# Performance work log

Hardware: AMD Instinct MI355X
Metric: run time of the kernel (lower is better)

## Reference

```python
import jax, jax.numpy as jnp
import numpy as np

D_MODEL = 1024
N_HEADS = 16
D_HEAD = D_MODEL // N_HEADS
BATCH = 2
SEQ = 2048


def setup_inputs() -> dict:
    key = jax.random.key(0)
    ks = jax.random.split(key, 16)
    s = 0.02
    d = D_MODEL
    return {
        "x": jax.random.normal(ks[0], (BATCH, SEQ, d), jnp.float32),
        "Wq": jax.random.normal(ks[1], (d, d), jnp.float32) * s,
        "bq": jnp.zeros((d,), jnp.float32),
        "Wk": jax.random.normal(ks[2], (d, d), jnp.float32) * s,
        "bk": jnp.zeros((d,), jnp.float32),
        "Wv": jax.random.normal(ks[3], (d, d), jnp.float32) * s,
        "bv": jnp.zeros((d,), jnp.float32),
        "Wo": jax.random.normal(ks[4], (d, d), jnp.float32) * s,
        "bo": jnp.zeros((d,), jnp.float32),
        "Wt": jax.random.normal(ks[5], (d, 1), jnp.float32) * s,
        "bt": jnp.zeros((1,), jnp.float32),
        "Wg": jax.random.normal(ks[6], (d, d), jnp.float32) * s,
        "bg": jnp.zeros((d,), jnp.float32),
    }


def _evolved_attention(x, Wq, bq, Wk, bk, Wv, bv, Wo, bo, Wt, bt, Wg, bg):
    B, S, D = x.shape
    H, dh = N_HEADS, D_HEAD

    def heads(y):  # [B,S,D] -> [B,H,S,dh]
        return y.reshape(B, S, H, dh).transpose(0, 2, 1, 3)

    q = heads(x @ Wq + bq)
    k = heads(x @ Wk + bk)
    v = heads(x @ Wv + bv)

    # cosine similarity (F.normalize with eps=1e-12)
    qn = q / jnp.maximum(jnp.linalg.norm(q, axis=-1, keepdims=True), 1e-12)
    kn = k / jnp.maximum(jnp.linalg.norm(k, axis=-1, keepdims=True), 1e-12)
    scores = jnp.einsum("bhqd,bhkd->bhqk", qn, kn)

    # adaptive temperature: sigmoid(temp_proj(mean_s x)) + 0.5, shape [B,1]
    temp = jax.nn.sigmoid(x.mean(axis=1) @ Wt + bt) + 0.5  # [B,1]
    scores = scores / temp[:, None, None, :]  # broadcast [B,1,1,1]

    # sparsemax-style: softmax over top-k (k = S//4), scattered back
    kk = max(1, S // 4)
    vals, idx = jax.lax.top_k(scores, kk)          # [B,H,S,kk]
    w = jax.nn.softmax(vals, axis=-1)
    rows = jnp.arange(B * H * S)[:, None]
    attn = (
        jnp.zeros((B * H * S, S), scores.dtype)
        .at[rows, idx.reshape(-1, kk)]
        .set(w.reshape(-1, kk))
        .reshape(B, H, S, S)
    )

    out = jnp.einsum("bhqk,bhkd->bhqd", attn, v)
    out = out.transpose(0, 2, 1, 3).reshape(B, S, D)
    out = out @ Wo + bo

    # highway gating
    gate = jax.nn.sigmoid(x @ Wg + bg)
    return gate * out + (1.0 - gate) * x


def reference(x, Wq, bq, Wk, bk, Wv, bv, Wo, bo, Wt, bt, Wg, bg):
    return _evolved_attention(x, Wq, bq, Wk, bk, Wv, bv, Wo, bo, Wt, bt, Wg, bg)
```

## Files before the change

### kernel.cpp

```cpp
#include <hip/hip_runtime.h>

typedef unsigned short u16;
typedef __attribute__((ext_vector_type(4))) float f32x4;
typedef __attribute__((ext_vector_type(8))) short bf16x8;
typedef __attribute__((ext_vector_type(4))) int i32x4;

#define BB 2
#define SS 2048
#define DD 1024
#define HH 16
#define DH 64
#define KK 512

#define OFF_SCAL  ((size_t)0)
#define OFF_WT    ((size_t)256)
#define OFF_XB    (OFF_WT + (size_t)5*1024*1024*2)
#define OFF_AO    OFF_XB
#define OFF_QH    (OFF_XB + (size_t)4096*1024*2)
#define OFF_QN    (OFF_QH + (size_t)4096*4096*2)
#define OFF_KN    (OFF_QN + (size_t)4096*1024*2)
#define OFF_VT    (OFF_KN + (size_t)4096*1024*2)

__device__ __forceinline__ float b2f(u16 u) { return __uint_as_float(((unsigned)u) << 16); }
__device__ __forceinline__ u16 f2b(float f) {
    unsigned u = __float_as_uint(f);
    return (u16)((u + 0x7fffu + ((u >> 16) & 1u)) >> 16);
}

__device__ __forceinline__ void gload16(const u16* g, u16* l) {
    __builtin_amdgcn_global_load_lds(
        (__attribute__((address_space(1))) void*)g,
        (__attribute__((address_space(3))) void*)l, 16, 0, 0);
}

__global__ __launch_bounds__(256) void convert_x(const float* x, u16* xb) {
    int i = (blockIdx.x * 256 + threadIdx.x) * 4;
    float4 v = *(const float4*)(x + i);
    u16 r0 = f2b(v.x), r1 = f2b(v.y), r2 = f2b(v.z), r3 = f2b(v.w);
    xb[i] = r0; xb[i + 1] = r1; xb[i + 2] = r2; xb[i + 3] = r3;
}

__global__ __launch_bounds__(256) void transpose_w(
        const float* Wq, const float* Wk, const float* Wv, const float* Wg, const float* Wo,
        u16* WT) {
    int z = blockIdx.z;
    const float* src = (z == 0) ? Wq : (z == 1) ? Wk : (z == 2) ? Wv : (z == 3) ? Wg : Wo;
    u16* dst = WT + (size_t)z * 1024 * 1024;
    __shared__ float tile[64][65];
    int n0 = blockIdx.x * 64, k0 = blockIdx.y * 64;
    int rbase = threadIdx.x >> 6, c = threadIdx.x & 63;
#pragma unroll
    for (int i = 0; i < 16; i++) {
        int r = i * 4 + rbase;
        tile[r][c] = src[(size_t)(k0 + r) * 1024 + n0 + c];
    }
    __syncthreads();
#pragma unroll
    for (int i = 0; i < 16; i++) {
        int r = i * 4 + rbase;
        dst[(size_t)(n0 + r) * 1024 + k0 + c] = f2b(tile[c][r]);
    }
}

__global__ __launch_bounds__(256) void temp_partial(const float* x, const float* Wt,
                                                    float* accbuf) {
    int b = blockIdx.x >> 5, ch = blockIdx.x & 31;
    float a = 0.f;
    for (int si = 0; si < 64; si++) {
        int s = ch * 64 + si;
        const float* xr = x + ((size_t)(b * SS + s)) * DD;
#pragma unroll
        for (int k = 0; k < 4; k++) {
            int c = threadIdx.x + k * 256;
            a += xr[c] * Wt[c];
        }
    }
    for (int o = 32; o; o >>= 1) a += __shfl_xor(a, o);
    __shared__ float red[4];
    if ((threadIdx.x & 63) == 0) red[threadIdx.x >> 6] = a;
    __syncthreads();
    if (threadIdx.x == 0) atomicAdd(&accbuf[b], red[0] + red[1] + red[2] + red[3]);
}

__global__ void temp_final(const float* accbuf, const float* bt, float* itemp) {
    int t = threadIdx.x;
    if (t < BB) {
        float v = accbuf[t] / (float)SS + bt[0];
        float tmp = 1.f / (1.f + __expf(-v)) + 0.5f;
        itemp[t] = 1.f / tmp;
    }
}

__global__ __launch_bounds__(256) void gemm_qkvg(
        const u16* X, const u16* WT,
        const float* bq, const float* bk, const float* bv, const float* bg, u16* Qh) {
    __shared__ __align__(16) u16 la[128 * 32];
    __shared__ __align__(16) u16 lb[128 * 32];
    int tid = threadIdx.x, wid = tid >> 6, lane = tid & 63;
    int quad = lane >> 4, ml = lane & 15;
    int m0 = blockIdx.x * 128, n0 = blockIdx.y * 128;
    int wr = wid >> 1, wc = wid & 1;

    f32x4 acc[4][4];
#pragma unroll
    for (int i = 0; i < 4; i++)
#pragma unroll
        for (int j = 0; j < 4; j++) acc[i][j] = (f32x4){0.f, 0.f, 0.f, 0.f};

    int t0 = wid * 2, t1 = t0 + 1;
    int r0 = lane >> 2, kp = lane & 3;
    const u16* ga0 = X + (size_t)(m0 + t0 * 16 + r0) * 1024 + kp * 8;
    const u16* ga1 = X + (size_t)(m0 + t1 * 16 + r0) * 1024 + kp * 8;
    const u16* gb0 = WT + (size_t)(n0 + t0 * 16 + r0) * 1024 + kp * 8;
    const u16* gb1 = WT + (size_t)(n0 + t1 * 16 + r0) * 1024 + kp * 8;
    u16* la0 = la + t0 * 512; u16* la1 = la + t1 * 512;
    u16* lb0 = lb + t0 * 512; u16* lb1 = lb + t1 * 512;

    for (int k0 = 0; k0 < 1024; k0 += 32) {
        gload16(ga0 + k0, la0);
        gload16(ga1 + k0, la1);
        gload16(gb0 + k0, lb0);
        gload16(gb1 + k0, lb1);
        __syncthreads();
        bf16x8 af[4], bfr[4];
#pragma unroll
        for (int mi = 0; mi < 4; mi++)
            af[mi] = *(const bf16x8*)&la[(wr * 64 + mi * 16 + ml) * 32 + quad * 8];
#pragma unroll
        for (int ni = 0; ni < 4; ni++)
            bfr[ni] = *(const bf16x8*)&lb[(wc * 64 + ni * 16 + ml) * 32 + quad * 8];
#pragma unroll
        for (int mi = 0; mi < 4; mi++)
#pragma unroll
            for (int ni = 0; ni < 4; ni++)
                acc[mi][ni] = __builtin_amdgcn_mfma_f32_16x16x32_bf16(af[mi], bfr[ni],
                                                                      acc[mi][ni], 0, 0, 0);
        __syncthreads();
    }

#pragma unroll
    for (int mi = 0; mi < 4; mi++)
#pragma unroll
        for (int ni = 0; ni < 4; ni++) {
            int col = n0 + wc * 64 + ni * 16 + ml;
            int mat = col >> 10, bc = col & 1023;
            const float* bp = (mat == 0) ? bq : (mat == 1) ? bk : (mat == 2) ? bv : bg;
            float bias = bp[bc];
#pragma unroll
            for (int r = 0; r < 4; r++) {
                int row = m0 + wr * 64 + mi * 16 + quad * 4 + r;
                Qh[(size_t)row * 4096 + col] = f2b(acc[mi][ni][r] + bias);
            }
        }
}

__global__ __launch_bounds__(256) void norm_repack(const u16* Qh, u16* qn, u16* kn, u16* vt) {
    int wid = threadIdx.x >> 6, lane = threadIdx.x & 63;
    int idx = blockIdx.x * 4 + wid;
    int token = idx >> 4, h = idx & 15;
    int b = token >> 11, s = token & 2047;
    int bh = b * HH + h;
    const u16* rowp = Qh + (size_t)token * 4096 + h * 64;
    float q = b2f(rowp[lane]);
    float k = b2f(rowp[1024 + lane]);
    u16 v = rowp[2048 + lane];
    float sq = q * q, sk = k * k;
    for (int o = 32; o; o >>= 1) { sq += __shfl_xor(sq, o); sk += __shfl_xor(sk, o); }
    float qd = fmaxf(sqrtf(sq), 1e-12f), kd = fmaxf(sqrtf(sk), 1e-12f);
    qn[((size_t)bh * SS + s) * DH + lane] = f2b(q / qd);
    kn[((size_t)bh * SS + s) * DH + lane] = f2b(k / kd);
    vt[((size_t)bh * DH + lane) * SS + s] = v;
}

#define EST 2088

__global__ __launch_bounds__(1024, 8) void attn_kernel(
        const u16* qn, const u16* kn, const u16* vt, const float* itemp, u16* ao) {
    __shared__ __align__(16) u16 e16[16 * EST];
    __shared__ float pvp[3][16][66];
    __shared__ float zrow_s[16];

    int tid = threadIdx.x, wid = tid >> 6, lane = tid & 63;
    int quad = lane >> 4, nl = lane & 15;
    int bh = blockIdx.x >> 7, qt = blockIdx.x & 127;
    int b = bh >> 4, h = bh & 15;
    const u16* qbase = qn + ((size_t)bh * SS + qt * 16) * DH;
    const u16* kbase = kn + (size_t)bh * SS * DH;
    const u16* vbase = vt + (size_t)bh * DH * SS;
    float it = itemp[b];

    bf16x8 aq0 = *(const bf16x8*)(qbase + nl * DH + quad * 8);
    bf16x8 aq1 = *(const bf16x8*)(qbase + nl * DH + 32 + quad * 8);

#pragma unroll 4
    for (int c = 0; c < 8; c++) {
        int j = c * 256 + wid * 16 + nl;
        const u16* kr = kbase + (size_t)j * DH;
        bf16x8 b0 = *(const bf16x8*)(kr + quad * 8);
        bf16x8 b1 = *(const bf16x8*)(kr + 32 + quad * 8);
        f32x4 acc = (f32x4){0.f, 0.f, 0.f, 0.f};
        acc = __builtin_amdgcn_mfma_f32_16x16x32_bf16(aq0, b0, acc, 0, 0, 0);
        acc = __builtin_amdgcn_mfma_f32_16x16x32_bf16(aq1, b1, acc, 0, 0, 0);
#pragma unroll
        for (int r = 0; r < 4; r++) e16[(quad * 4 + r) * EST + j] = f2b(acc[r] * it);
    }
    __syncthreads();

    {
        int row = wid;
        u16* rp = &e16[row * EST];
        int kk[32];
#pragma unroll
        for (int i = 0; i < 4; i++) {
            i32x4 kv = *(const i32x4*)(rp + i * 512 + lane * 8);
#pragma unroll
            for (int j = 0; j < 4; j++) {
                int r2 = kv[j];
                int t = ((r2 >> 15) & 0x00010001) * 0x7FFF;
                int key2 = r2 ^ 0x80008000 ^ t;
                kk[i * 8 + j * 2]     = key2 & 0xFFFF;
                kk[i * 8 + j * 2 + 1] = ((unsigned)key2) >> 16;
            }
        }
#pragma unroll
        for (int c = 0; c < 32; c++) asm volatile("" : "+v"(kk[c]));

        int P = 0;
        for (int bit = 15; bit >= 0; bit--) {
            int cand = P | (1 << bit);
            int cnt = 0;
#pragma unroll
            for (int c = 0; c < 32; c++)
                cnt += (int)__popcll(__ballot(kk[c] >= cand));
            if (cnt >= KK) P = cand;
            if (cnt == KK) break;
        }

        float z = 0.f;
#pragma unroll
        for (int i = 0; i < 4; i++) {
            i32x4 ev;
#pragma unroll
            for (int j = 0; j < 4; j++) {
                int k0i = kk[i * 8 + j * 2], k1i = kk[i * 8 + j * 2 + 1];
                unsigned r0 = (unsigned)k0i ^ ((k0i & 0x8000) ? 0x8000u : 0xFFFFu);
                unsigned r1 = (unsigned)k1i ^ ((k1i & 0x8000) ? 0x8000u : 0xFFFFu);
                float f0 = __uint_as_float(r0 << 16);
                float f1 = __uint_as_float(r1 << 16);
                float e0 = (k0i >= P) ? __expf(f0) : 0.f;
                float e1 = (k1i >= P) ? __expf(f1) : 0.f;
                z += e0 + e1;
                int pk;
                asm("v_cvt_pk_bf16_f32 %0, %1, %2" : "=v"(pk) : "v"(e0), "v"(e1));
                ev[j] = pk;
            }
            *(i32x4*)(rp + i * 512 + lane * 8) = ev;
        }
#pragma unroll
        for (int o = 32; o; o >>= 1) z += __shfl_xor(z, o);
        if (lane == 0) zrow_s[row] = z;
    }
    __syncthreads();

    f32x4 accp = (f32x4){0.f, 0.f, 0.f, 0.f};
    int kq = wid >> 2, g = wid & 3;
    int dh = g * 16 + nl;
    const u16* vrow = vbase + (size_t)dh * SS;
#pragma unroll 4
    for (int c = 0; c < 8; c++) {
        int j0 = kq * 512 + c * 64;
#pragma unroll
        for (int ks = 0; ks < 2; ks++) {
            bf16x8 a = *(const bf16x8*)&e16[nl * EST + j0 + ks * 32 + quad * 8];
            bf16x8 bfr = *(const bf16x8*)(vrow + j0 + ks * 32 + quad * 8);
            accp = __builtin_amdgcn_mfma_f32_16x16x32_bf16(a, bfr, accp, 0, 0, 0);
        }
    }
    if (kq) {
#pragma unroll
        for (int r = 0; r < 4; r++) pvp[kq - 1][quad * 4 + r][dh] = accp[r];
    }
    __syncthreads();
    if (kq == 0) {
#pragma unroll
        for (int r = 0; r < 4; r++) {
            int q = quad * 4 + r;
            float val = (accp[r] + pvp[0][q][dh] + pvp[1][q][dh] + pvp[2][q][dh]) / zrow_s[q];
            size_t row = (size_t)(b * SS + qt * 16 + q);
            ao[row * DD + h * 64 + dh] = f2b(val);
        }
    }
}

__global__ __launch_bounds__(256) void gemm_out(
        const u16* AO, const u16* WTo, const float* bo,
        const u16* Qh, const float* x, float* out) {
    __shared__ __align__(16) u16 la[128 * 32];
    __shared__ __align__(16) u16 lb[128 * 32];
    int tid = threadIdx.x, wid = tid >> 6, lane = tid & 63;
    int quad = lane >> 4, ml = lane & 15;
    int m0 = blockIdx.x * 128, n0 = blockIdx.y * 128;
    int wr = wid >> 1, wc = wid & 1;

    f32x4 acc[4][4];
#pragma unroll
    for (int i = 0; i < 4; i++)
#pragma unroll
        for (int j = 0; j < 4; j++) acc[i][j] = (f32x4){0.f, 0.f, 0.f, 0.f};

    int t0 = wid * 2, t1 = t0 + 1;
    int r0 = lane >> 2, kp = lane & 3;
    const u16* ga0 = AO + (size_t)(m0 + t0 * 16 + r0) * 1024 + kp * 8;
    const u16* ga1 = AO + (size_t)(m0 + t1 * 16 + r0) * 1024 + kp * 8;
    const u16* gb0 = WTo + (size_t)(n0 + t0 * 16 + r0) * 1024 + kp * 8;
    const u16* gb1 = WTo + (size_t)(n0 + t1 * 16 + r0) * 1024 + kp * 8;
    u16* la0 = la + t0 * 512; u16* la1 = la + t1 * 512;
    u16* lb0 = lb + t0 * 512; u16* lb1 = lb + t1 * 512;

    for (int k0 = 0; k0 < 1024; k0 += 32) {
        gload16(ga0 + k0, la0);
        gload16(ga1 + k0, la1);
        gload16(gb0 + k0, lb0);
        gload16(gb1 + k0, lb1);
        __syncthreads();
        bf16x8 af[4], bfr[4];
#pragma unroll
        for (int mi = 0; mi < 4; mi++)
            af[mi] = *(const bf16x8*)&la[(wr * 64 + mi * 16 + ml) * 32 + quad * 8];
#pragma unroll
        for (int ni = 0; ni < 4; ni++)
            bfr[ni] = *(const bf16x8*)&lb[(wc * 64 + ni * 16 + ml) * 32 + quad * 8];
#pragma unroll
        for (int mi = 0; mi < 4; mi++)
#pragma unroll
            for (int ni = 0; ni < 4; ni++)
                acc[mi][ni] = __builtin_amdgcn_mfma_f32_16x16x32_bf16(af[mi], bfr[ni],
                                                                      acc[mi][ni], 0, 0, 0);
        __syncthreads();
    }

#pragma unroll
    for (int mi = 0; mi < 4; mi++)
#pragma unroll
        for (int ni = 0; ni < 4; ni++) {
            int col = n0 + wc * 64 + ni * 16 + ml;
            float bias = bo[col];
#pragma unroll
            for (int r = 0; r < 4; r++) {
                int row = m0 + wr * 64 + mi * 16 + quad * 4 + r;
                float gv = b2f(Qh[(size_t)row * 4096 + 3072 + col]);
                float gate = 1.f / (1.f + __expf(-gv));
                float xv = x[(size_t)row * 1024 + col];
                float o = acc[mi][ni][r] + bias;
                out[(size_t)row * 1024 + col] = gate * o + (1.f - gate) * xv;
            }
        }
}

extern "C" void kernel_launch(void* const* d_in, const int* in_sizes, int n_in,
                              void* d_out, int out_size, void* d_ws, size_t ws_size,
                              hipStream_t stream) {
    const float* x  = (const float*)d_in[0];
    const float* Wq = (const float*)d_in[1];
    const float* bq = (const float*)d_in[2];
    const float* Wk = (const float*)d_in[3];
    const float* bk = (const float*)d_in[4];
    const float* Wv = (const float*)d_in[5];
    const float* bv = (const float*)d_in[6];
    const float* Wo = (const float*)d_in[7];
    const float* bo = (const float*)d_in[8];
    const float* Wt = (const float*)d_in[9];
    const float* bt = (const float*)d_in[10];
    const float* Wg = (const float*)d_in[11];
    const float* bg = (const float*)d_in[12];

    char* w = (char*)d_ws;
    float* accbuf = (float*)(w + OFF_SCAL);
    float* itemp  = accbuf + 2;
    u16*   WT     = (u16*)(w + OFF_WT);
    u16*   xb     = (u16*)(w + OFF_XB);
    u16*   ao     = (u16*)(w + OFF_AO);
    u16*   Qh     = (u16*)(w + OFF_QH);
    u16*   qn     = (u16*)(w + OFF_QN);
    u16*   kn     = (u16*)(w + OFF_KN);
    u16*   vt     = (u16*)(w + OFF_VT);

    hipMemsetAsync(accbuf, 0, 2 * sizeof(float), stream);

    convert_x<<<4096, 256, 0, stream>>>(x, xb);
    transpose_w<<<dim3(16, 16, 5), 256, 0, stream>>>(Wq, Wk, Wv, Wg, Wo, WT);
    temp_partial<<<64, 256, 0, stream>>>(x, Wt, accbuf);
    temp_final<<<1, 64, 0, stream>>>(accbuf, bt, itemp);
    gemm_qkvg<<<dim3(32, 32), 256, 0, stream>>>(xb, WT, bq, bk, bv, bg, Qh);
    norm_repack<<<16384, 256, 0, stream>>>(Qh, qn, kn, vt);
    attn_kernel<<<4096, 1024, 0, stream>>>(qn, kn, vt, itemp, ao);
    gemm_out<<<dim3(32, 8), 256, 0, stream>>>(ao, WT + (size_t)4 * 1024 * 1024, bo, Qh, x,
                                              (float*)d_out);
}
```

Before: 510.6 us.

## Swizzle attention block order, raise MFMA priority, split radix-select popcount chains

Remaps block IDs so consecutive blocks are spread across XCDs (stride 512), which changes which (batch, head) K/V data each XCD's L2 serves. Wraps the MFMA instructions in s_setprio so matrix-core waves get higher scheduling priority. The radix-select count loop now uses four independent accumulators to shorten the dependency chain, and the keys are pinned in registers through explicit v_mov. These are several small scheduling tweaks; the swizzle may hurt or help L2 locality depending on how the hardware dispatches blocks.

```diff
diff --git a/kernel.cpp b/kernel.cpp
--- a/kernel.cpp
+++ b/kernel.cpp
@@ -182,7 +182,9 @@
 
     int tid = threadIdx.x, wid = tid >> 6, lane = tid & 63;
     int quad = lane >> 4, nl = lane & 15;
-    int bh = blockIdx.x >> 7, qt = blockIdx.x & 127;
+    int bid = blockIdx.x;
+    int swz = (bid & 7) * 512 + (bid >> 3);
+    int bh = swz >> 7, qt = swz & 127;
     int b = bh >> 4, h = bh & 15;
     const u16* qbase = qn + ((size_t)bh * SS + qt * 16) * DH;
     const u16* kbase = kn + (size_t)bh * SS * DH;
@@ -199,39 +201,44 @@
         bf16x8 b0 = *(const bf16x8*)(kr + quad * 8);
         bf16x8 b1 = *(const bf16x8*)(kr + 32 + quad * 8);
         f32x4 acc = (f32x4){0.f, 0.f, 0.f, 0.f};
+        __builtin_amdgcn_s_setprio(1);
         acc = __builtin_amdgcn_mfma_f32_16x16x32_bf16(aq0, b0, acc, 0, 0, 0);
         acc = __builtin_amdgcn_mfma_f32_16x16x32_bf16(aq1, b1, acc, 0, 0, 0);
+        __builtin_amdgcn_s_setprio(0);
 #pragma unroll
         for (int r = 0; r < 4; r++) e16[(quad * 4 + r) * EST + j] = f2b(acc[r] * it);
     }
     __syncthreads();
 
     {
-        int row = wid;
-        u16* rp = &e16[row * EST];
+        u16* rp = &e16[wid * EST];
         int kk[32];
 #pragma unroll
         for (int i = 0; i < 4; i++) {
             i32x4 kv = *(const i32x4*)(rp + i * 512 + lane * 8);
 #pragma unroll
             for (int j = 0; j < 4; j++) {
-                int r2 = kv[j];
-                int t = ((r2 >> 15) & 0x00010001) * 0x7FFF;
-                int key2 = r2 ^ 0x80008000 ^ t;
-                kk[i * 8 + j * 2]     = key2 & 0xFFFF;
-                kk[i * 8 + j * 2 + 1] = ((unsigned)key2) >> 16;
+                unsigned r2 = (unsigned)kv[j];
+                unsigned t = ((r2 >> 15) & 0x00010001u) * 0x7FFFu;
+                unsigned key2 = r2 ^ 0x80008000u ^ t;
+                int lo = (int)(key2 & 0xFFFFu), hi = (int)(key2 >> 16);
+                asm volatile("v_mov_b32 %0, %1" : "=v"(kk[i * 8 + j * 2]) : "v"(lo));
+                asm volatile("v_mov_b32 %0, %1" : "=v"(kk[i * 8 + j * 2 + 1]) : "v"(hi));
             }
         }
-#pragma unroll
-        for (int c = 0; c < 32; c++) asm volatile("" : "+v"(kk[c]));
 
         int P = 0;
         for (int bit = 15; bit >= 0; bit--) {
             int cand = P | (1 << bit);
-            int cnt = 0;
-#pragma unroll
-            for (int c = 0; c < 32; c++)
-                cnt += (int)__popcll(__ballot(kk[c] >= cand));
+            int c0 = 0, c1 = 0, c2 = 0, c3 = 0;
+#pragma unroll
+            for (int c = 0; c < 32; c += 4) {
+                c0 += (int)__popcll(__ballot(kk[c] >= cand));
+                c1 += (int)__popcll(__ballot(kk[c + 1] >= cand));
+                c2 += (int)__popcll(__ballot(kk[c + 2] >= cand));
+                c3 += (int)__popcll(__ballot(kk[c + 3] >= cand));
+            }
+            int cnt = (c0 + c1) + (c2 + c3);
             if (cnt >= KK) P = cand;
             if (cnt == KK) break;
         }
@@ -250,15 +257,15 @@
                 float e0 = (k0i >= P) ? __expf(f0) : 0.f;
                 float e1 = (k1i >= P) ? __expf(f1) : 0.f;
                 z += e0 + e1;
-                int pk;
-                asm("v_cvt_pk_bf16_f32 %0, %1, %2" : "=v"(pk) : "v"(e0), "v"(e1));
-                ev[j] = pk;
+                int pw;
+                asm("v_cvt_pk_bf16_f32 %0, %1, %2" : "=v"(pw) : "v"(e0), "v"(e1));
+                ev[j] = pw;
             }
             *(i32x4*)(rp + i * 512 + lane * 8) = ev;
         }
 #pragma unroll
         for (int o = 32; o; o >>= 1) z += __shfl_xor(z, o);
-        if (lane == 0) zrow_s[row] = z;
+        if (lane == 0) zrow_s[wid] = z;
     }
     __syncthreads();
 
@@ -273,7 +280,9 @@
         for (int ks = 0; ks < 2; ks++) {
             bf16x8 a = *(const bf16x8*)&e16[nl * EST + j0 + ks * 32 + quad * 8];
             bf16x8 bfr = *(const bf16x8*)(vrow + j0 + ks * 32 + quad * 8);
+            __builtin_amdgcn_s_setprio(1);
             accp = __builtin_amdgcn_mfma_f32_16x16x32_bf16(a, bfr, accp, 0, 0, 0);
+            __builtin_amdgcn_s_setprio(0);
         }
     }
     if (kq) {
```

New measurement: 499.8 us. 1.02x faster.
